# Kernel tuning notes

Hardware: AMD Instinct MI355X
Metric: run time of the kernel (lower is better)

## Reference

```python
import jax, jax.numpy as jnp
import numpy as np

V, E, H, T = 50000, 1024, 1024, 128
L, MAXL = 50, 50
PAD, O_TOK = 0, 1


def setup_inputs() -> dict:
    key = jax.random.key(0)
    ks = jax.random.split(key, 18)
    s = 0.05
    f = lambda k, shape: jax.random.normal(k, shape, jnp.float32) * s
    return {
        'input_ids': jax.random.randint(ks[0], (1, L), 1, V),
        'tag_ids': jax.random.randint(ks[1], (1, L), 1, T),  # >=1 so no pad tags
        'word_embed': f(ks[2], (V, E)),
        'enc_Wih': f(ks[3], (3 * H, E)),
        'enc_Whh': f(ks[4], (3 * H, H)),
        'enc_bih': f(ks[5], (3 * H,)),
        'enc_bhh': f(ks[6], (3 * H,)),
        'dec_embed': f(ks[7], (T, H)),
        'attn_W': f(ks[8], (MAXL, 2 * H)),
        'attn_b': f(ks[9], (MAXL,)),
        'comb_W': f(ks[10], (H, 2 * H)),
        'comb_b': f(ks[11], (H,)),
        'dec_Wih': f(ks[12], (3 * H, H)),
        'dec_Whh': f(ks[13], (3 * H, H)),
        'dec_bih': f(ks[14], (3 * H,)),
        'dec_bhh': f(ks[15], (3 * H,)),
        'out_W': f(ks[16], (T, H)),
        'out_b': f(ks[17], (T,)),
    }


def _gru_cell(x, h, Wih, Whh, bih, bhh):
    # PyTorch GRU cell semantics
    gi = Wih @ x + bih
    gh = Whh @ h + bhh
    i_r, i_z, i_n = jnp.split(gi, 3)
    h_r, h_z, h_n = jnp.split(gh, 3)
    r = jax.nn.sigmoid(i_r + h_r)
    z = jax.nn.sigmoid(i_z + h_z)
    n = jnp.tanh(i_n + r * h_n)
    return (1.0 - z) * n + z * h


def _forward(word_embed, enc_Wih, enc_Whh, enc_bih, enc_bhh,
             dec_embed, attn_W, attn_b, comb_W, comb_b,
             dec_Wih, dec_Whh, dec_bih, dec_bhh, out_W, out_b,
             input_ids, tag_ids):
    src = input_ids[0]  # (L,)
    tgt = tag_ids[0]    # (L,)

    def enc_step(h, tok):
        h2 = _gru_cell(word_embed[tok], h, enc_Wih, enc_Whh, enc_bih, enc_bhh)
        return h2, h2

    h_enc, enc_outs = jax.lax.scan(enc_step, jnp.zeros((H,), word_embed.dtype), src)
    # enc_outs: (L, H); L == MAX_LENGTH so the buffer is fully filled

    dec_in = jnp.concatenate([jnp.array([O_TOK], tgt.dtype), tgt[:-1]])  # teacher forcing

    def dec_step(h, xt):
        tok, tgt_t = xt
        e = dec_embed[tok]  # (H,), dropout is identity in eval
        aw = jax.nn.softmax(attn_W @ jnp.concatenate([e, h]) + attn_b)  # (MAXL,)
        ctx = aw @ enc_outs  # (H,)
        o = jax.nn.relu(comb_W @ jnp.concatenate([e, ctx]) + comb_b)
        h2 = _gru_cell(o, h, dec_Wih, dec_Whh, dec_bih, dec_bhh)
        logp = jax.nn.log_softmax(out_W @ h2 + out_b)  # decoder output (log-probs)
        # original applies CrossEntropyLoss on log-probs -> log_softmax applied twice
        nll = -jax.nn.log_softmax(logp)[tgt_t]
        step_loss = jnp.where(tgt_t == PAD, jnp.zeros((), logp.dtype), nll)
        return h2, (logp, step_loss)

    _, (logps, losses) = jax.lax.scan(dec_step, h_enc, (dec_in, tgt))
    return logps, jnp.sum(losses)  # (L, T), scalar


def reference(input_ids, tag_ids, word_embed, enc_Wih, enc_Whh, enc_bih, enc_bhh,
              dec_embed, attn_W, attn_b, comb_W, comb_b,
              dec_Wih, dec_Whh, dec_bih, dec_bhh, out_W, out_b):
    return _forward(word_embed, enc_Wih, enc_Whh, enc_bih, enc_bhh,
                    dec_embed, attn_W, attn_b, comb_W, comb_b,
                    dec_Wih, dec_Whh, dec_bih, dec_bhh, out_W, out_b,
                    input_ids, tag_ids)
```

## Files before the change

kernel.cpp:

```cpp
#include <hip/hip_runtime.h>
#include <cstdint>


#define HDIM 1024
#define LSEQ 50
#define TDIM 128
#define G3   3072
#define PB   6
#define NPROD 128
#define LSTRP 65

typedef float f32x4 __attribute__((ext_vector_type(4)));
typedef _Float16 h2 __attribute__((ext_vector_type(2)));

#if __has_builtin(__builtin_amdgcn_fdot2)
#define FDOT2(a,b,c) __builtin_amdgcn_fdot2((a),(b),(c),false)
#else
__device__ __forceinline__ float fdot2_sw(h2 a, h2 b, float c){
  return c + (float)a[0]*(float)b[0] + (float)a[1]*(float)b[1];
}
#define FDOT2(a,b,c) fdot2_sw((a),(b),(c))
#endif

struct KArgs {
  const int* input_ids; const int* tag_ids;
  const float* word_embed;
  const float* enc_Wih; const float* enc_Whh; const float* enc_bih; const float* enc_bhh;
  const float* dec_embed; const float* attn_W; const float* attn_b;
  const float* comb_W; const float* comb_b;
  const float* dec_Wih; const float* dec_Whh; const float* dec_bih; const float* dec_bhh;
  const float* out_W; const float* out_b;
  float* out;
  unsigned* ctrP; unsigned* ctrE; unsigned* ctrM; unsigned* ctrO; unsigned* ctrV;
  float* hbE;
  float* hbD;
  float* obD;
  float* logits;
  float* GI;
  float* attn_e;
  float* pre_comb;
  float* MT;
  float* enc_outs;
};

__device__ __forceinline__ void fence_vm(){
  asm volatile("s_waitcnt vmcnt(0)" ::: "memory");
}
__device__ __forceinline__ void st_coh(float* p, float v){
  __hip_atomic_store(p, v, __ATOMIC_RELAXED, __HIP_MEMORY_SCOPE_AGENT);
}
__device__ __forceinline__ void st_tag(float* p, float v, unsigned tag){
  unsigned b = (__float_as_uint(v) & ~31u) | tag;
  st_coh(p, __uint_as_float(b));
}
__device__ __forceinline__ void stf(unsigned* p, unsigned v){
  __hip_atomic_store(p, v, __ATOMIC_RELAXED, __HIP_MEMORY_SCOPE_AGENT);
}
__device__ __forceinline__ unsigned ldu(const unsigned* p){
  return __hip_atomic_load(p, __ATOMIC_RELAXED, __HIP_MEMORY_SCOPE_AGENT);
}
__device__ __forceinline__ void addc(unsigned* base, int bid){
  __hip_atomic_fetch_add(base + (bid&7)*16, 1u, __ATOMIC_RELAXED, __HIP_MEMORY_SCOPE_AGENT);
}
__device__ __forceinline__ void addc0(unsigned* base){
  __hip_atomic_fetch_add(base, 1u, __ATOMIC_RELAXED, __HIP_MEMORY_SCOPE_AGENT);
}
__device__ __forceinline__ f32x4 coh_load4(const float* p){
  f32x4 v;
  asm volatile("global_load_dwordx4 %0, %1, off sc0 sc1\n\ts_waitcnt vmcnt(0)"
               : "=v"(v) : "v"(p) : "memory");
  return v;
}

template<int N>
__device__ __forceinline__ void wred_batch(float* v){
  #pragma unroll
  for(int o=32;o>0;o>>=1){
    #pragma unroll
    for(int i=0;i<N;i++) v[i] += __shfl_xor(v[i],o,64);
  }
}
__device__ __forceinline__ float wred_sum(float v){
  #pragma unroll
  for(int o=32;o>0;o>>=1) v += __shfl_xor(v,o,64);
  return v;
}
__device__ __forceinline__ float wred_max(float v){
  #pragma unroll
  for(int o=32;o>0;o>>=1) v = fmaxf(v,__shfl_xor(v,o,64));
  return v;
}

struct Chunk { f32x4 a,b,c,d; };
__device__ __forceinline__ Chunk load_chunk(const float* __restrict__ row, int lane){
  const f32x4* p = reinterpret_cast<const f32x4*>(row) + lane*4;
  Chunk w; w.a=p[0]; w.b=p[1]; w.c=p[2]; w.d=p[3]; return w;
}
__device__ __forceinline__ float chunk_dot(const Chunk& w, const float* hc){
  return w.a.x*hc[0]+w.a.y*hc[1]+w.a.z*hc[2]+w.a.w*hc[3]
       + w.b.x*hc[4]+w.b.y*hc[5]+w.b.z*hc[6]+w.b.w*hc[7]
       + w.c.x*hc[8]+w.c.y*hc[9]+w.c.z*hc[10]+w.c.w*hc[11]
       + w.d.x*hc[12]+w.d.y*hc[13]+w.d.z*hc[14]+w.d.w*hc[15];
}
__device__ __forceinline__ void load_vec16(const float* __restrict__ v, float* hc, int lane){
  const f32x4* p = reinterpret_cast<const f32x4*>(v) + lane*4;
  f32x4 x0=p[0],x1=p[1],x2=p[2],x3=p[3];
  hc[0]=x0.x; hc[1]=x0.y; hc[2]=x0.z; hc[3]=x0.w;
  hc[4]=x1.x; hc[5]=x1.y; hc[6]=x1.z; hc[7]=x1.w;
  hc[8]=x2.x; hc[9]=x2.y; hc[10]=x2.z; hc[11]=x2.w;
  hc[12]=x3.x; hc[13]=x3.y; hc[14]=x3.z; hc[15]=x3.w;
}

struct PChunk { unsigned m[8]; };
__device__ __forceinline__ h2 as_h2(unsigned u){ return __builtin_bit_cast(h2, u); }
__device__ __forceinline__ unsigned as_u(h2 h){ return __builtin_bit_cast(unsigned, h); }
__device__ __forceinline__ unsigned pack2(float a, float b){
  return as_u((h2){(_Float16)a, (_Float16)b});
}
__device__ __forceinline__ PChunk load_pchunk(const float* __restrict__ row, int lane){
  const f32x4* p = reinterpret_cast<const f32x4*>(row) + lane*4;
  f32x4 a=p[0],b=p[1],c=p[2],d=p[3];
  PChunk w;
  w.m[0]=pack2(a.x,a.y); w.m[1]=pack2(a.z,a.w);
  w.m[2]=pack2(b.x,b.y); w.m[3]=pack2(b.z,b.w);
  w.m[4]=pack2(c.x,c.y); w.m[5]=pack2(c.z,c.w);
  w.m[6]=pack2(d.x,d.y); w.m[7]=pack2(d.z,d.w);
  return w;
}
__device__ __forceinline__ void pinp(PChunk& c){
  asm volatile("" : "+v"(c.m[0]),"+v"(c.m[1]),"+v"(c.m[2]),"+v"(c.m[3]),
                    "+v"(c.m[4]),"+v"(c.m[5]),"+v"(c.m[6]),"+v"(c.m[7]));
}
__device__ __forceinline__ void pin32(unsigned& x){ asm volatile("" : "+v"(x)); }
__device__ __forceinline__ float pdot(const PChunk& w, const h2* hp){
  float acc = 0.f;
  #pragma unroll
  for(int k=0;k<8;k++) acc = FDOT2(as_h2(w.m[k]), hp[k], acc);
  return acc;
}
__device__ __forceinline__ float sigm(float x){ return 1.f/(1.f+expf(-x)); }

template<int SLP>
__device__ __forceinline__ void stage_tag_p(h2* ldsp, const float* g, int tid, unsigned tag){
  const float* p = g + 4*tid;
  f32x4 v;
  for(;;){
    v = coh_load4(p);
    unsigned m = ((__float_as_uint(v.x)&31u)^tag) | ((__float_as_uint(v.y)&31u)^tag)
               | ((__float_as_uint(v.z)&31u)^tag) | ((__float_as_uint(v.w)&31u)^tag);
    if(m==0u) break;
    if(SLP) __builtin_amdgcn_s_sleep(SLP);
  }
  int q = tid>>2, m0 = (tid&3)*2;
  ldsp[m0*LSTRP+q]     = (h2){(_Float16)v.x,(_Float16)v.y};
  ldsp[(m0+1)*LSTRP+q] = (h2){(_Float16)v.z,(_Float16)v.w};
}
__device__ __forceinline__ void read8p(const h2* ldsp, h2* hp, int lane){
  #pragma unroll
  for(int k=0;k<8;k++) hp[k]=ldsp[k*LSTRP+lane];
}
__device__ __forceinline__ float hread(const h2* ldsp, int j){
  int pj = j>>1;
  h2 v = ldsp[(pj&7)*LSTRP + (pj>>3)];
  return (float)v[j&1];
}

__device__ __forceinline__ void wait8(const unsigned* base, unsigned n, int lane){
  const unsigned* p = base + lane*16;
  for(;;){
    unsigned v = (lane<8)? ldu(p) : 0xFFFFFFFFu;
    if(__all((int)(v>=n))) return;
    __builtin_amdgcn_s_sleep(8);
  }
}

__global__ __launch_bounds__(256,1) void seq2seq_kernel(KArgs A){
  const int bid = blockIdx.x, tid = threadIdx.x;
  const int wave = tid>>6, lane = tid&63;
  __shared__ h2 ldsp_h[8*LSTRP+8];
  __shared__ h2 ldsp_o[8*LSTRP+8];
  __shared__ h2 awpL[32];
  __shared__ float smr[64];
  __shared__ float smL[TDIM];
  __shared__ float smA[64];

  const int gv = bid*4 + wave;

  {
    const int r0 = gv*3;
    Chunk w0 = load_chunk(A.enc_Wih + (size_t)r0*HDIM, lane);
    Chunk w1 = load_chunk(A.enc_Wih + (size_t)(r0+1)*HDIM, lane);
    Chunk w2 = load_chunk(A.enc_Wih + (size_t)(r0+2)*HDIM, lane);
    float b0=A.enc_bih[r0], b1=A.enc_bih[r0+1], b2=A.enc_bih[r0+2];
    for(int te=0;te<LSEQ;++te){
      int tok = A.input_ids[te];
      float ec[16]; load_vec16(A.word_embed + (size_t)tok*HDIM, ec, lane);
      float d[3];
      d[0]=chunk_dot(w0,ec); d[1]=chunk_dot(w1,ec); d[2]=chunk_dot(w2,ec);
      wred_batch<3>(d);
      if(lane==0){
        st_coh(&A.GI[te*G3+r0],   d[0]+b0);
        st_coh(&A.GI[te*G3+r0+1], d[1]+b1);
        st_coh(&A.GI[te*G3+r0+2], d[2]+b2);
      }
    }
    Chunk wc = load_chunk(A.comb_W + (size_t)gv*2*HDIM, lane);
    float bc = A.comb_b[gv];
    Chunk wa; wa.a=0.f; wa.b=0.f; wa.c=0.f; wa.d=0.f;
    float ba = 0.f;
    if(gv < LSEQ){ wa = load_chunk(A.attn_W + (size_t)gv*2*HDIM, lane); ba = A.attn_b[gv]; }
    for(int t=0;t<LSEQ;++t){
      int tok = (t==0)?1:A.tag_ids[t-1];
      float ec[16]; load_vec16(A.dec_embed + (size_t)tok*HDIM, ec, lane);
      float d[2];
      d[0]=chunk_dot(wc,ec);
      d[1]=(gv<LSEQ)? chunk_dot(wa,ec) : 0.f;
      wred_batch<2>(d);
      if(lane==0){
        st_coh(&A.pre_comb[t*HDIM+gv], d[0]+bc);
        if(gv<LSEQ) st_coh(&A.attn_e[t*LSEQ+gv], d[1]+ba);
      }
    }
  }
  fence_vm();
  __syncthreads();
  if(tid==0) addc(A.ctrP, bid);
  if(wave==0) wait8(A.ctrP, 32u, lane);
  __syncthreads();

  const int p = bid - PB;
  const bool is_prod = (p>=0 && p<NPROD);
  const int base = is_prod ? p*8 : 0;
  const int j8 = base + (tid&7);

  if(is_prod){
    PChunk wep[6];
    #pragma unroll
    for(int i=0;i<6;i++){
      int r = wave + 4*i;
      int le=r/3, g=r-3*le, row=g*HDIM+base+le;
      wep[i] = load_pchunk(A.enc_Whh + (size_t)row*HDIM, lane);
      pinp(wep[i]);
    }
    float bh0=A.enc_bhh[j8], bh1=A.enc_bhh[HDIM+j8], bh2=A.enc_bhh[2*HDIM+j8];
    for(int te=0;te<LSEQ;++te){
      const float* GIr = A.GI + te*G3;
      float gi0=GIr[j8], gi1=GIr[HDIM+j8], gi2=GIr[2*HDIM+j8];
      h2 hp[8];
      if(te>0){
        stage_tag_p<1>(ldsp_h, A.hbE + ((te-1)&1)*HDIM, tid, (unsigned)(te&31));
        __syncthreads();
        read8p(ldsp_h, hp, lane);
      } else {
        #pragma unroll
        for(int k=0;k<8;k++) hp[k]=(h2){(_Float16)0.f,(_Float16)0.f};
      }
      float part[6];
      #pragma unroll
      for(int i=0;i<6;i++) part[i]=pdot(wep[i],hp);
      wred_batch<6>(part);
      if(lane==0){
        #pragma unroll
        for(int i=0;i<6;i++) smr[wave+4*i]=part[i];
      }
      __syncthreads();
      if(tid<8){
        int j = base+tid;
        float gr=smr[tid*3]+bh0, gz=smr[tid*3+1]+bh1, gn=smr[tid*3+2]+bh2;
        float hj = (te>0)? hread(ldsp_h, j) : 0.f;
        float r_=sigm(gi0+gr), z_=sigm(gi1+gz);
        float n_=tanhf(gi2+r_*gn);
        float h2v=(1.f-z_)*n_+z_*hj;
        st_tag(&A.hbE[(te&1)*HDIM+j], h2v, (unsigned)((te+1)&31));
        st_coh(&A.enc_outs[te*HDIM+j], h2v);
        if(te==LSEQ-1) st_tag(&A.hbD[j], h2v, 0u);
      }
      __syncthreads();
    }
    fence_vm();
    __syncthreads();
    if(tid==0) addc(A.ctrE, bid);
  }
  if(wave==0) wait8(A.ctrE, 16u, lane);
  __syncthreads();

  {
    Chunk wm = load_chunk(A.comb_W + (size_t)gv*2*HDIM + HDIM, lane);
    for(int sg=0;sg<10;++sg){
      float pt[5];
      #pragma unroll
      for(int j=0;j<5;j++){
        float ec[16]; load_vec16(A.enc_outs + (sg*5+j)*HDIM, ec, lane);
        pt[j]=chunk_dot(wm,ec);
      }
      wred_batch<5>(pt);
      if(lane==0){
        #pragma unroll
        for(int j=0;j<5;j++) st_coh(&A.MT[(sg*5+j)*HDIM+gv], pt[j]);
      }
    }
  }
  fence_vm();
  __syncthreads();
  if(tid==0) addc(A.ctrM, bid);
  {
    const bool keep = is_prod || bid<5 || (bid>=134 && bid<150);
    if(!keep) return;
  }
  if(wave==0) wait8(A.ctrM, 32u, lane);
  __syncthreads();

  if(bid < 4){
    const int oi = bid*256 + tid;
    PChunk wa13[13];
    int srow[13];
    #pragma unroll
    for(int i=0;i<13;i++){
      int s = wave + 4*i; int sc = (s<LSEQ)? s : 0;
      wa13[i] = load_pchunk(A.attn_W + (size_t)sc*2*HDIM + HDIM, lane);
      pinp(wa13[i]);
      srow[i] = s;
    }
    unsigned mp[25];
    #pragma unroll
    for(int k=0;k<25;k++){
      mp[k] = pack2(A.MT[(2*k)*HDIM+oi], A.MT[(2*k+1)*HDIM+oi]);
      pin32(mp[k]);
    }
    for(int t=0;t<LSEQ;++t){
      const unsigned tg = (unsigned)(t&31);
      float ae[13];
      #pragma unroll
      for(int i=0;i<13;i++)
        ae[i] = (srow[i]<LSEQ)? A.attn_e[t*LSEQ+srow[i]] : 0.f;
      float pcv = A.pre_comb[t*HDIM+oi];
      stage_tag_p<1>(ldsp_h, A.hbD + (t%3)*HDIM, tid, tg);
      __syncthreads();
      h2 hp[8]; read8p(ldsp_h, hp, lane);
      float pl[13];
      #pragma unroll
      for(int i=0;i<13;i++) pl[i]=pdot(wa13[i],hp);
      wred_batch<13>(pl);
      if(lane==0){
        #pragma unroll
        for(int i=0;i<13;i++) if(srow[i]<LSEQ) smL[srow[i]]=pl[i]+ae[i];
      }
      __syncthreads();
      if(wave==0){
        float l = (lane<LSEQ)? smL[lane] : -1e30f;
        float m = wred_max(l);
        float pe = (lane<LSEQ)? expf(l-m) : 0.f;
        float ss = wred_sum(pe);
        if(lane<LSEQ) smA[lane] = pe/ss;
      }
      __syncthreads();
      if(tid<25) awpL[tid] = (h2){(_Float16)smA[2*tid],(_Float16)smA[2*tid+1]};
      __syncthreads();
      float acc = pcv;
      #pragma unroll
      for(int k=0;k<25;k++) acc = FDOT2(as_h2(mp[k]), awpL[k], acc);
      st_tag(&A.obD[(t&1)*HDIM+oi], fmaxf(acc,0.f), tg);
      __syncthreads();
    }
  } else if(bid == 4){
    float loss = 0.f;
    for(int t=0;t<LSEQ;++t){
      if(tid<32){
        const float* pp = A.logits + (t&1)*TDIM + 4*tid;
        const unsigned tg = (unsigned)(t&31);
        f32x4 v;
        for(;;){
          v = coh_load4(pp);
          unsigned m = ((__float_as_uint(v.x)&31u)^tg) | ((__float_as_uint(v.y)&31u)^tg)
                     | ((__float_as_uint(v.z)&31u)^tg) | ((__float_as_uint(v.w)&31u)^tg);
          if(m==0u) break;
          __builtin_amdgcn_s_sleep(2);
        }
        smL[4*tid]=v.x; smL[4*tid+1]=v.y; smL[4*tid+2]=v.z; smL[4*tid+3]=v.w;
      }
      __syncthreads();
      if(tid==0) stf(A.ctrV, (unsigned)(t+1));
      if(wave==0){
        float l0=smL[lane], l1=smL[lane+64];
        float m  = wred_max(fmaxf(l0,l1));
        float pe = expf(l0-m)+expf(l1-m);
        float s1 = wred_sum(pe);
        float lse = m + logf(s1);
        float lp0 = l0-lse, lp1 = l1-lse;
        float m2  = wred_max(fmaxf(lp0,lp1));
        float p2  = expf(lp0-m2)+expf(lp1-m2);
        float s2  = wred_sum(p2);
        float lse2 = m2 + logf(s2);
        A.out[t*TDIM + lane]      = lp0;
        A.out[t*TDIM + 64 + lane] = lp1;
        int tg2 = A.tag_ids[t];
        float c = ((lane==tg2)?(lse2-lp0):0.f) + ((lane+64==tg2)?(lse2-lp1):0.f);
        c = wred_sum(c);
        if(tg2 != 0) loss += c;
      }
      __syncthreads();
    }
    if(tid==0) A.out[LSEQ*TDIM] = loss;
  } else if(is_prod){
    PChunk whp[6], wip[6];
    #pragma unroll
    for(int i=0;i<6;i++){
      int r = wave + 4*i;
      int le=r/3, g=r-3*le, row=g*HDIM+base+le;
      whp[i] = load_pchunk(A.dec_Whh + (size_t)row*HDIM, lane);
      pinp(whp[i]);
      wip[i] = load_pchunk(A.dec_Wih + (size_t)row*HDIM, lane);
      pinp(wip[i]);
    }
    float dh0=A.dec_bhh[j8], dh1=A.dec_bhh[HDIM+j8], dh2=A.dec_bhh[2*HDIM+j8];
    float di0=A.dec_bih[j8], di1=A.dec_bih[HDIM+j8], di2=A.dec_bih[2*HDIM+j8];
    for(int t=0;t<LSEQ;++t){
      const unsigned tg = (unsigned)(t&31);
      stage_tag_p<1>(ldsp_h, A.hbD + (t%3)*HDIM, tid, tg);
      __syncthreads();
      h2 hp[8]; read8p(ldsp_h, hp, lane);
      float ph[6];
      #pragma unroll
      for(int i=0;i<6;i++) ph[i]=pdot(whp[i],hp);
      wred_batch<6>(ph);
      if(lane==0){
        #pragma unroll
        for(int i=0;i<6;i++) smr[wave+4*i]=ph[i];
      }
      if(wave==0 && t>=3){
        const unsigned tgt = 16u*(unsigned)(t-2);
        for(;;){
          unsigned v = (lane==0)? ldu(A.ctrO) : tgt;
          if(__all((int)(v>=tgt))) break;
          __builtin_amdgcn_s_sleep(2);
        }
      }
      stage_tag_p<1>(ldsp_o, A.obD + (t&1)*HDIM, tid, tg);
      __syncthreads();
      h2 op[8]; read8p(ldsp_o, op, lane);
      float po[6];
      #pragma unroll
      for(int i=0;i<6;i++) po[i]=pdot(wip[i],op);
      wred_batch<6>(po);
      if(lane==0){
        #pragma unroll
        for(int i=0;i<6;i++) smr[32+wave+4*i]=po[i];
      }
      __syncthreads();
      if(tid<8){
        int j = base+tid;
        float gr=smr[tid*3]+dh0,    gz=smr[tid*3+1]+dh1,    gn=smr[tid*3+2]+dh2;
        float ir=smr[32+tid*3]+di0, iz=smr[32+tid*3+1]+di1, inn=smr[32+tid*3+2]+di2;
        float hj = hread(ldsp_h, j);
        float r_=sigm(ir+gr), z_=sigm(iz+gz);
        float n_=tanhf(inn+r_*gn);
        float h2v=(1.f-z_)*n_+z_*hj;
        st_tag(&A.hbD[((t+1)%3)*HDIM+j], h2v, (unsigned)((t+1)&31));
      }
      __syncthreads();
    }
  } else {
    const int ob = bid-134;
    PChunk wop[2];
    float bo[2];
    #pragma unroll
    for(int i=0;i<2;i++){
      int row = ob*8 + wave*2 + i;
      wop[i]=load_pchunk(A.out_W+(size_t)row*HDIM,lane);
      pinp(wop[i]);
      bo[i]=A.out_b[row];
    }
    for(int t=0;t<LSEQ;++t){
      const unsigned tg1 = (unsigned)((t+1)&31);
      stage_tag_p<2>(ldsp_h, A.hbD + ((t+1)%3)*HDIM, tid, tg1);
      __syncthreads();
      if(tid==0) addc0(A.ctrO);
      h2 hp[8]; read8p(ldsp_h, hp, lane);
      float pt[2]={pdot(wop[0],hp),pdot(wop[1],hp)};
      wred_batch<2>(pt);
      if(wave==0 && t>=2){
        const unsigned tgt = (unsigned)(t-1);
        for(;;){
          unsigned v = (lane==0)? ldu(A.ctrV) : tgt;
          if(__all((int)(v>=tgt))) break;
          __builtin_amdgcn_s_sleep(4);
        }
      }
      __syncthreads();
      if(lane==0){
        int row = ob*8 + wave*2;
        st_tag(&A.logits[(t&1)*TDIM + row],   pt[0]+bo[0], (unsigned)(t&31));
        st_tag(&A.logits[(t&1)*TDIM + row+1], pt[1]+bo[1], (unsigned)(t&31));
      }
      __syncthreads();
    }
  }
}

extern "C" void kernel_launch(void* const* d_in, const int* in_sizes, int n_in,
                              void* d_out, int out_size, void* d_ws, size_t ws_size,
                              hipStream_t stream){
  (void)in_sizes; (void)n_in; (void)out_size; (void)ws_size;
  KArgs A;
  A.input_ids = (const int*)d_in[0];
  A.tag_ids   = (const int*)d_in[1];
  A.word_embed= (const float*)d_in[2];
  A.enc_Wih   = (const float*)d_in[3];
  A.enc_Whh   = (const float*)d_in[4];
  A.enc_bih   = (const float*)d_in[5];
  A.enc_bhh   = (const float*)d_in[6];
  A.dec_embed = (const float*)d_in[7];
  A.attn_W    = (const float*)d_in[8];
  A.attn_b    = (const float*)d_in[9];
  A.comb_W    = (const float*)d_in[10];
  A.comb_b    = (const float*)d_in[11];
  A.dec_Wih   = (const float*)d_in[12];
  A.dec_Whh   = (const float*)d_in[13];
  A.dec_bih   = (const float*)d_in[14];
  A.dec_bhh   = (const float*)d_in[15];
  A.out_W     = (const float*)d_in[16];
  A.out_b     = (const float*)d_in[17];
  A.out       = (float*)d_out;

  unsigned* u = (unsigned*)d_ws;
  A.ctrP = u;
  A.ctrE = u + 128;
  A.ctrM = u + 256;
  A.ctrO = u + 384;
  A.ctrV = u + 448;
  float* f = (float*)d_ws + 1024;
  A.hbE    = f; f += 2*HDIM;
  A.hbD    = f; f += 3*HDIM;
  A.obD    = f; f += 2*HDIM;
  A.logits = f; f += 2*TDIM;
  A.GI       = f; f += LSEQ*G3;
  A.attn_e   = f; f += LSEQ*LSEQ + 14;
  A.pre_comb = f; f += LSEQ*HDIM;
  A.MT       = f; f += LSEQ*HDIM;
  A.enc_outs = f; f += LSEQ*HDIM;

  (void)hipMemsetAsync(d_ws, 0, 4096, stream);
  (void)hipMemsetAsync((char*)d_ws + 4096, 0xFF, 7424*4, stream);
  void* args[] = { &A };
  hipError_t err = hipLaunchCooperativeKernel((const void*)seq2seq_kernel,
                                              dim3(256), dim3(256), args, 0, stream);
  if(err != hipSuccess){
    hipLaunchKernelGGL(seq2seq_kernel, dim3(256), dim3(256), 0, stream, A);
  }
}
```

Measured before the change: 511.2 us.

## Compute encoder input projections locally in producer blocks, drop the global barrier

Each producer block now computes the enc_Wih·x projections for exactly the gate rows it later consumes, keeping them in shared memory instead of a global GI buffer. This removes the grid-wide ctrP barrier and the global round trip for GI. The precompute of comb and attention rows for decoder embeddings moves to the 128 non-producer blocks, which run concurrently with the encoder recurrence. Input projections now use fp16 packed dot products, which lowers precision. The encoder's start is delayed by each producer's own 50-step projection loop.

```diff
diff --git a/kernel.cpp b/kernel.cpp
--- a/kernel.cpp
+++ b/kernel.cpp
@@ -5,7 +5,6 @@
 #define HDIM 1024
 #define LSEQ 50
 #define TDIM 128
-#define G3   3072
 #define PB   6
 #define NPROD 128
 #define LSTRP 65
@@ -31,12 +30,11 @@
   const float* dec_Wih; const float* dec_Whh; const float* dec_bih; const float* dec_bhh;
   const float* out_W; const float* out_b;
   float* out;
-  unsigned* ctrP; unsigned* ctrE; unsigned* ctrM; unsigned* ctrO; unsigned* ctrV;
+  unsigned* ctrE; unsigned* ctrM; unsigned* ctrO; unsigned* ctrV;
   float* hbE;
   float* hbD;
   float* obD;
   float* logits;
-  float* GI;
   float* attn_e;
   float* pre_comb;
   float* MT;
@@ -139,6 +137,10 @@
   return acc;
 }
 __device__ __forceinline__ float sigm(float x){ return 1.f/(1.f+expf(-x)); }
+__device__ __forceinline__ void pack16(const float* ec, h2* ep){
+  #pragma unroll
+  for(int k=0;k<8;k++) ep[k]=(h2){(_Float16)ec[2*k],(_Float16)ec[2*k+1]};
+}
 
 template<int SLP>
 __device__ __forceinline__ void stage_tag_p(h2* ldsp, const float* g, int tid, unsigned tag){
@@ -183,50 +185,9 @@
   __shared__ float smr[64];
   __shared__ float smL[TDIM];
   __shared__ float smA[64];
+  __shared__ float giL[LSEQ*24];
 
   const int gv = bid*4 + wave;
-
-  {
-    const int r0 = gv*3;
-    Chunk w0 = load_chunk(A.enc_Wih + (size_t)r0*HDIM, lane);
-    Chunk w1 = load_chunk(A.enc_Wih + (size_t)(r0+1)*HDIM, lane);
-    Chunk w2 = load_chunk(A.enc_Wih + (size_t)(r0+2)*HDIM, lane);
-    float b0=A.enc_bih[r0], b1=A.enc_bih[r0+1], b2=A.enc_bih[r0+2];
-    for(int te=0;te<LSEQ;++te){
-      int tok = A.input_ids[te];
-      float ec[16]; load_vec16(A.word_embed + (size_t)tok*HDIM, ec, lane);
-      float d[3];
-      d[0]=chunk_dot(w0,ec); d[1]=chunk_dot(w1,ec); d[2]=chunk_dot(w2,ec);
-      wred_batch<3>(d);
-      if(lane==0){
-        st_coh(&A.GI[te*G3+r0],   d[0]+b0);
-        st_coh(&A.GI[te*G3+r0+1], d[1]+b1);
-        st_coh(&A.GI[te*G3+r0+2], d[2]+b2);
-      }
-    }
-    Chunk wc = load_chunk(A.comb_W + (size_t)gv*2*HDIM, lane);
-    float bc = A.comb_b[gv];
-    Chunk wa; wa.a=0.f; wa.b=0.f; wa.c=0.f; wa.d=0.f;
-    float ba = 0.f;
-    if(gv < LSEQ){ wa = load_chunk(A.attn_W + (size_t)gv*2*HDIM, lane); ba = A.attn_b[gv]; }
-    for(int t=0;t<LSEQ;++t){
-      int tok = (t==0)?1:A.tag_ids[t-1];
-      float ec[16]; load_vec16(A.dec_embed + (size_t)tok*HDIM, ec, lane);
-      float d[2];
-      d[0]=chunk_dot(wc,ec);
-      d[1]=(gv<LSEQ)? chunk_dot(wa,ec) : 0.f;
-      wred_batch<2>(d);
-      if(lane==0){
-        st_coh(&A.pre_comb[t*HDIM+gv], d[0]+bc);
-        if(gv<LSEQ) st_coh(&A.attn_e[t*LSEQ+gv], d[1]+ba);
-      }
-    }
-  }
-  fence_vm();
-  __syncthreads();
-  if(tid==0) addc(A.ctrP, bid);
-  if(wave==0) wait8(A.ctrP, 32u, lane);
-  __syncthreads();
 
   const int p = bid - PB;
   const bool is_prod = (p>=0 && p<NPROD);
@@ -234,6 +195,31 @@
   const int j8 = base + (tid&7);
 
   if(is_prod){
+    {
+      PChunk wgi[6]; float bgi[6];
+      #pragma unroll
+      for(int i=0;i<6;i++){
+        int r = wave + 4*i;
+        int le=r/3, g=r-3*le, grow=g*HDIM+base+le;
+        wgi[i] = load_pchunk(A.enc_Wih + (size_t)grow*HDIM, lane);
+        pinp(wgi[i]);
+        bgi[i] = A.enc_bih[grow];
+      }
+      for(int te=0;te<LSEQ;++te){
+        int tok = A.input_ids[te];
+        float ec[16]; load_vec16(A.word_embed + (size_t)tok*HDIM, ec, lane);
+        h2 ep[8]; pack16(ec, ep);
+        float d[6];
+        #pragma unroll
+        for(int i=0;i<6;i++) d[i]=pdot(wgi[i],ep);
+        wred_batch<6>(d);
+        if(lane==0){
+          #pragma unroll
+          for(int i=0;i<6;i++) giL[te*24 + wave+4*i] = d[i]+bgi[i];
+        }
+      }
+      __syncthreads();
+    }
     PChunk wep[6];
     #pragma unroll
     for(int i=0;i<6;i++){
@@ -244,8 +230,6 @@
     }
     float bh0=A.enc_bhh[j8], bh1=A.enc_bhh[HDIM+j8], bh2=A.enc_bhh[2*HDIM+j8];
     for(int te=0;te<LSEQ;++te){
-      const float* GIr = A.GI + te*G3;
-      float gi0=GIr[j8], gi1=GIr[HDIM+j8], gi2=GIr[2*HDIM+j8];
       h2 hp[8];
       if(te>0){
         stage_tag_p<1>(ldsp_h, A.hbE + ((te-1)&1)*HDIM, tid, (unsigned)(te&31));
@@ -267,6 +251,7 @@
       if(tid<8){
         int j = base+tid;
         float gr=smr[tid*3]+bh0, gz=smr[tid*3+1]+bh1, gn=smr[tid*3+2]+bh2;
+        float gi0=giL[te*24+3*tid], gi1=giL[te*24+3*tid+1], gi2=giL[te*24+3*tid+2];
         float hj = (te>0)? hread(ldsp_h, j) : 0.f;
         float r_=sigm(gi0+gr), z_=sigm(gi1+gz);
         float n_=tanhf(gi2+r_*gn);
@@ -280,10 +265,46 @@
     fence_vm();
     __syncthreads();
     if(tid==0) addc(A.ctrE, bid);
-  }
+  } else {
+    const int q = (bid<6)? bid : bid-128;
+    PChunk wpc[2]; float bpc[2]; int ri[2];
+    #pragma unroll
+    for(int k=0;k<2;k++){
+      ri[k] = q*8 + wave*2 + k;
+      wpc[k] = load_pchunk(A.comb_W + (size_t)ri[k]*2*HDIM, lane);
+      pinp(wpc[k]);
+      bpc[k] = A.comb_b[ri[k]];
+    }
+    for(int t=0;t<LSEQ;++t){
+      int tok = (t==0)?1:A.tag_ids[t-1];
+      float ec[16]; load_vec16(A.dec_embed + (size_t)tok*HDIM, ec, lane);
+      h2 ep[8]; pack16(ec, ep);
+      float d[2] = {pdot(wpc[0],ep), pdot(wpc[1],ep)};
+      wred_batch<2>(d);
+      if(lane==0){
+        st_coh(&A.pre_comb[t*HDIM+ri[0]], d[0]+bpc[0]);
+        st_coh(&A.pre_comb[t*HDIM+ri[1]], d[1]+bpc[1]);
+      }
+    }
+    if(q < LSEQ){
+      PChunk wae = load_pchunk(A.attn_W + (size_t)q*2*HDIM, lane);
+      float bae = A.attn_b[q];
+      const int t0 = wave*13, tc = (wave<3)?13:11;
+      for(int u=0;u<tc;++u){
+        int t = t0+u;
+        int tok = (t==0)?1:A.tag_ids[t-1];
+        float ec[16]; load_vec16(A.dec_embed + (size_t)tok*HDIM, ec, lane);
+        h2 ep[8]; pack16(ec, ep);
+        float d = wred_sum(pdot(wae,ep));
+        if(lane==0) st_coh(&A.attn_e[t*LSEQ+q], d+bae);
+      }
+    }
+    fence_vm();
+    __syncthreads();
+  }
+
   if(wave==0) wait8(A.ctrE, 16u, lane);
   __syncthreads();
-
   {
     Chunk wm = load_chunk(A.comb_W + (size_t)gv*2*HDIM + HDIM, lane);
     for(int sg=0;sg<10;++sg){
@@ -523,17 +544,15 @@
   A.out       = (float*)d_out;
 
   unsigned* u = (unsigned*)d_ws;
-  A.ctrP = u;
-  A.ctrE = u + 128;
-  A.ctrM = u + 256;
-  A.ctrO = u + 384;
-  A.ctrV = u + 448;
+  A.ctrE = u;
+  A.ctrM = u + 128;
+  A.ctrO = u + 256;
+  A.ctrV = u + 320;
   float* f = (float*)d_ws + 1024;
   A.hbE    = f; f += 2*HDIM;
   A.hbD    = f; f += 3*HDIM;
   A.obD    = f; f += 2*HDIM;
   A.logits = f; f += 2*TDIM;
-  A.GI       = f; f += LSEQ*G3;
   A.attn_e   = f; f += LSEQ*LSEQ + 14;
   A.pre_comb = f; f += LSEQ*HDIM;
   A.MT       = f; f += LSEQ*HDIM;
```

Measured after the change: 463.9 us. -9.3%, faster.
